# Performance work log

Measured on AMD Instinct MI355X. Metric: run time of the kernel, lower is better.

The kernel has to match this reference:

```python
import jax, jax.numpy as jnp
import numpy as np

EPS = 1e-6
LAMBDA_INIT = 0.8
ROPE_BASE = 10000.0
NUM_HEADS = 8


def rmsnorm(x, w):
    rms = jnp.sqrt(jnp.mean(x * x, axis=-1, keepdims=True) + EPS)
    return x / rms * w


def apply_rope(x):
    # Faithful to source: positions are taken along dim -2 of x.
    # Here x has shape (B, r, H, d), so rotation angle is indexed by HEAD index
    # (this mirrors the original torch code, where apply_rope is called on
    # (B, seq, H, d) tensors and uses x.shape[-2] == H for positions).
    d = x.shape[-1]
    half = d // 2  # d is even (head_dim=64)
    pos = jnp.arange(x.shape[-2])
    dim_idx = jnp.arange(half, dtype=x.dtype)
    freqs = 1.0 / (ROPE_BASE ** (dim_idx / half))
    angles = pos[:, None].astype(jnp.float32) * freqs  # (H, half)
    cos, sin = jnp.cos(angles), jnp.sin(angles)
    x1, x2 = x[..., :half], x[..., half:2 * half]
    return jnp.concatenate([x1 * cos - x2 * sin, x1 * sin + x2 * cos], axis=-1)


def linterp(x, out_size):
    # torch F.interpolate(mode='linear', align_corners=False) along axis 1 of (B, L, C)
    in_size = x.shape[1]
    scale = in_size / out_size
    coords = jnp.clip((jnp.arange(out_size) + 0.5) * scale - 0.5, 0.0, in_size - 1)
    lo = jnp.floor(coords).astype(jnp.int32)
    hi = jnp.minimum(lo + 1, in_size - 1)
    w = (coords - lo)[None, :, None].astype(x.dtype)
    return x[:, lo] * (1 - w) + x[:, hi] * w


def setup_inputs() -> dict:
    key = jax.random.key(0)
    ks = jax.random.split(key, 12)
    B, L, C = 4, 4096, 1024
    H = NUM_HEADS
    d = C // (2 * H)  # 64
    s = 0.02
    return {
        "x": jax.random.normal(ks[0], (B, L, C), jnp.float32),
        "Wq": jax.random.normal(ks[1], (C, C), jnp.float32) * s,
        "Wk": jax.random.normal(ks[2], (C, C), jnp.float32) * s,
        "Wv": jax.random.normal(ks[3], (C, C), jnp.float32) * s,
        "Wo": jax.random.normal(ks[4], (C, C), jnp.float32) * s,
        "q_norm_w": 1.0 + jax.random.normal(ks[5], (d,), jnp.float32) * s,
        "k_norm_w": 1.0 + jax.random.normal(ks[6], (d,), jnp.float32) * s,
        "head_norm_w": 1.0 + jax.random.normal(ks[7], (2 * d,), jnp.float32) * s,
        "lambda_q1": jax.random.normal(ks[8], (d,), jnp.float32) * 0.1,
        "lambda_k1": jax.random.normal(ks[9], (d,), jnp.float32) * 0.1,
        "lambda_q2": jax.random.normal(ks[10], (d,), jnp.float32) * 0.1,
        "lambda_k2": jax.random.normal(ks[11], (d,), jnp.float32) * 0.1,
    }


def reference(x, Wq, Wk, Wv, Wo, q_norm_w, k_norm_w, head_norm_w,
              lambda_q1, lambda_k1, lambda_q2, lambda_k2):
    B, L, C = x.shape
    H = NUM_HEADS
    d = C // (2 * H)
    scale = d ** -0.5
    r = max(1, int(L ** 0.75))  # 512 for L=4096

    xd = linterp(x, r)  # (B, r, C)

    q = (xd @ Wq.T).reshape(B, r, H, 2, d)
    k = (xd @ Wk.T).reshape(B, r, H, 2, d)
    v = (xd @ Wv.T).reshape(B, r, H, 2 * d)

    q1 = apply_rope(rmsnorm(q[..., 0, :], q_norm_w))
    q2 = apply_rope(rmsnorm(q[..., 1, :], q_norm_w))
    k1 = apply_rope(rmsnorm(k[..., 0, :], k_norm_w))
    k2 = apply_rope(rmsnorm(k[..., 1, :], k_norm_w))

    # (B, H, r, d)
    q1, q2 = jnp.swapaxes(q1, 1, 2), jnp.swapaxes(q2, 1, 2)
    k1, k2 = jnp.swapaxes(k1, 1, 2), jnp.swapaxes(k2, 1, 2)
    v = jnp.swapaxes(v, 1, 2)  # (B, H, r, 2d)

    lam = (jnp.exp(jnp.sum(lambda_q1 * lambda_k1))
           - jnp.exp(jnp.sum(lambda_q2 * lambda_k2)) + LAMBDA_INIT)

    attn1 = jax.nn.softmax(jnp.einsum('bhqd,bhkd->bhqk', q1, k1) * scale, axis=-1)
    attn2 = jax.nn.softmax(jnp.einsum('bhqd,bhkd->bhqk', q2, k2) * scale, axis=-1)
    diff = jnp.einsum('bhqk,bhkd->bhqd', attn1 - lam * attn2, v)  # (B,H,r,2d)

    diff = jnp.swapaxes(diff, 1, 2)  # (B, r, H, 2d)
    diff = rmsnorm(diff, head_norm_w) * (1.0 - LAMBDA_INIT)
    lowrank_out = jax.nn.silu(diff.reshape(B, r, C) @ Wo.T)
    full_out = linterp(lowrank_out, L)
    return (full_out, lowrank_out)
```

## Files before the change

### kernel.cpp

```cpp
#include <hip/hip_runtime.h>

typedef __bf16 bf16_t;
typedef __bf16 bf16x8 __attribute__((ext_vector_type(8)));
typedef __bf16 bf16x4 __attribute__((ext_vector_type(4)));
typedef float  f32x4  __attribute__((ext_vector_type(4)));

#define MFMA16(a,b,c) __builtin_amdgcn_mfma_f32_16x16x32_bf16((a),(b),(c),0,0,0)

#define NB 4
#define LL 4096
#define CC 1024
#define HH 8
#define RR 512

__global__ void k_prep(const float* __restrict__ x,
                       const float* __restrict__ w0, const float* __restrict__ w1,
                       const float* __restrict__ w2, const float* __restrict__ w3,
                       bf16_t* __restrict__ wbf, bf16_t* __restrict__ xd) {
  int bid = blockIdx.x;
  if (bid < 4096) {
    int y = bid >> 10;
    const float* src = (y == 0) ? w0 : (y == 1) ? w1 : (y == 2) ? w2 : w3;
    int idx = (bid & 1023) * 256 + threadIdx.x;
    f32x4 v = *(const f32x4*)&src[(size_t)idx * 4];
    bf16x4 o;
#pragma unroll
    for (int j = 0; j < 4; ++j) o[j] = (bf16_t)v[j];
    *(bf16x4*)&wbf[(size_t)y * 1048576 + (size_t)idx * 4] = o;
  } else {
    int idx = (bid - 4096) * 256 + threadIdx.x;
    int c4  = idx & 255;
    int row = idx >> 8;
    int b = row >> 9, i = row & 511;
    const float* p0 = x + (size_t)(b * LL + 8 * i + 3) * CC + c4 * 4;
    f32x4 a = *(const f32x4*)p0;
    f32x4 bb = *(const f32x4*)(p0 + CC);
    bf16x4 o;
#pragma unroll
    for (int j = 0; j < 4; ++j) o[j] = (bf16_t)(0.5f * (a[j] + bb[j]));
    *(bf16x4*)&xd[(size_t)row * CC + c4 * 4] = o;
  }
}

template <int CH>
__device__ __forceinline__ void stage_async(const bf16_t* __restrict__ g, bf16_t* __restrict__ s, int t) {
#pragma unroll
  for (int j = 0; j < CH; ++j) {
    int c = t + j * 256;
    const bf16_t* ga = g + (c >> 2) * 1024 + (c & 3) * 8;
    bf16_t* la = s + c * 8;
    __builtin_amdgcn_global_load_lds((const __attribute__((address_space(1))) void*)ga,
                                     (__attribute__((address_space(3))) void*)la, 16, 0, 0);
  }
}

template <int MODE, int BM>
__global__ __launch_bounds__(256) void k_gemm(const bf16_t* __restrict__ A,
                                              const bf16_t* __restrict__ wbf,
                                              const float* __restrict__ qw,
                                              const float* __restrict__ kw,
                                              bf16_t* __restrict__ q1, bf16_t* __restrict__ q2,
                                              bf16_t* __restrict__ k1, bf16_t* __restrict__ k2,
                                              bf16_t* __restrict__ vt, float* __restrict__ outF) {
  __shared__ bf16_t sA[3][BM * 32];
  __shared__ bf16_t sB[3][128 * 32];
  const int z = (MODE == 0) ? blockIdx.z : 3;
  const bf16_t* W = wbf + (size_t)z * (1u << 20);
  int t = threadIdx.x;
  int lane = t & 63, w = t >> 6;
  int wr = w >> 1, wc = w & 1;
  int lr = lane & 15, quad = lane >> 4;
  int m0 = blockIdx.y * BM, n0 = blockIdx.x * 128;
  constexpr int NI = BM / 32;
  f32x4 acc[NI][4] = {};

  const bf16_t* Ab = A + (size_t)m0 * 1024;
  const bf16_t* Wb = W + (size_t)n0 * 1024;

  stage_async<BM / 64>(Ab, sA[0], t);
  stage_async<2>(Wb, sB[0], t);
  stage_async<BM / 64>(Ab + 32, sA[1], t);
  stage_async<2>(Wb + 32, sB[1], t);

  int cur = 0, stg = 2;
#pragma unroll 1
  for (int it = 0; it < 32; ++it) {
    if (it < 31) {
      if constexpr (BM == 128) asm volatile("s_waitcnt vmcnt(4) lgkmcnt(0)" ::: "memory");
      else                     asm volatile("s_waitcnt vmcnt(3) lgkmcnt(0)" ::: "memory");
    } else {
      asm volatile("s_waitcnt vmcnt(0) lgkmcnt(0)" ::: "memory");
    }
    __builtin_amdgcn_s_barrier();
    if (it < 30) {
      stage_async<BM / 64>(Ab + (it + 2) * 32, sA[stg], t);
      stage_async<2>(Wb + (it + 2) * 32, sB[stg], t);
    }
    const bf16_t* cA = sA[cur];
    const bf16_t* cB = sB[cur];
    bf16x8 af[NI], bfr[4];
#pragma unroll
    for (int i = 0; i < NI; ++i) af[i] = *(const bf16x8*)&cA[(wr * (BM / 2) + i * 16 + lr) * 32 + quad * 8];
#pragma unroll
    for (int j = 0; j < 4; ++j) bfr[j] = *(const bf16x8*)&cB[(wc * 64 + j * 16 + lr) * 32 + quad * 8];
#pragma unroll
    for (int i = 0; i < NI; ++i)
#pragma unroll
      for (int j = 0; j < 4; ++j)
        acc[i][j] = MFMA16(af[i], bfr[j], acc[i][j]);
    cur = (cur == 2) ? 0 : cur + 1;
    stg = (stg == 2) ? 0 : stg + 1;
  }

  if (MODE == 1) {
#pragma unroll
    for (int i = 0; i < NI; ++i)
#pragma unroll
      for (int j = 0; j < 4; ++j) {
        int row0 = m0 + wr * (BM / 2) + i * 16 + quad * 4;
        int col  = n0 + wc * 64 + j * 16 + lr;
#pragma unroll
        for (int rg = 0; rg < 4; ++rg) {
          float v = acc[i][j][rg];
          outF[(size_t)(row0 + rg) * 1024 + col] = v / (1.f + __expf(-v));
        }
      }
    return;
  }

  if (z == 2) {
#pragma unroll
    for (int i = 0; i < NI; ++i)
#pragma unroll
      for (int j = 0; j < 4; ++j) {
        int row0 = m0 + wr * (BM / 2) + i * 16 + quad * 4;
        int col  = n0 + wc * 64 + j * 16 + lr;
        int b = row0 >> 9, ii = row0 & 511;
        int h = col >> 7, nn = col & 127;
        bf16x4 pk;
#pragma unroll
        for (int rg = 0; rg < 4; ++rg) pk[rg] = (bf16_t)acc[i][j][rg];
        *(bf16x4*)&vt[(size_t)((b * HH + h) * 128 + nn) * 512 + ii] = pk;
      }
    return;
  }

  {
    const float* nw = z ? kw : qw;
    int colbase = n0 + wc * 64;
    int h = colbase >> 7;
    int slot = (colbase >> 6) & 1;
    bf16_t* dst = (z == 0) ? (slot ? q2 : q1) : (slot ? k2 : k1);
    float qs = (z == 0) ? 0.125f : 1.0f;
    float w0 = nw[lr], w1 = nw[16 + lr], w2 = nw[32 + lr], w3 = nw[48 + lr];
    const float nlog = -13.287712379549449f / 32.f;
    float f0 = exp2f((float)lr * nlog);
    float f1 = exp2f((float)(16 + lr) * nlog);
    float sn0, cs0, sn1, cs1;
    __sincosf((float)h * f0, &sn0, &cs0);
    __sincosf((float)h * f1, &sn1, &cs1);
#pragma unroll
    for (int i = 0; i < NI; ++i) {
#pragma unroll
      for (int rg = 0; rg < 4; ++rg) {
        float v0 = acc[i][0][rg], v1 = acc[i][1][rg], v2 = acc[i][2][rg], v3 = acc[i][3][rg];
        float ss = v0 * v0 + v1 * v1 + v2 * v2 + v3 * v3;
#pragma unroll
        for (int m = 1; m <= 8; m <<= 1) ss += __shfl_xor(ss, m);
        float rinv = qs / sqrtf(ss * (1.f / 64.f) + 1e-6f);
        float n0v = v0 * rinv * w0, n1v = v1 * rinv * w1, n2v = v2 * rinv * w2, n3v = v3 * rinv * w3;
        float o0 = n0v * cs0 - n2v * sn0;
        float o1 = n1v * cs1 - n3v * sn1;
        float o2 = n0v * sn0 + n2v * cs0;
        float o3 = n1v * sn1 + n3v * cs1;
        int row = m0 + wr * (BM / 2) + i * 16 + quad * 4 + rg;
        int b = row >> 9, seq = row & 511;
        size_t base = ((size_t)((b * HH + h) * RR + seq)) * 64;
        dst[base + lr]      = (bf16_t)o0;
        dst[base + 16 + lr] = (bf16_t)o1;
        dst[base + 32 + lr] = (bf16_t)o2;
        dst[base + 48 + lr] = (bf16_t)o3;
      }
    }
  }
}

__global__ __launch_bounds__(256) void k_attn(const bf16_t* __restrict__ q1, const bf16_t* __restrict__ q2,
                                              const bf16_t* __restrict__ k1, const bf16_t* __restrict__ k2,
                                              const bf16_t* __restrict__ vt,
                                              const float* __restrict__ lq1, const float* __restrict__ lk1,
                                              const float* __restrict__ lq2, const float* __restrict__ lk2,
                                              const float* __restrict__ hw, bf16_t* __restrict__ anorm) {
  __shared__ bf16_t P[16 * 520];
  __shared__ float Sm1[4][16], Sl1[4][16], Sm2[4][16], Sl2[4][16], Sq[4][16];
  int t = threadIdx.x;
  int lane = t & 63, w = t >> 6;
  int lr = lane & 15, quad = lane >> 4;
  int qt = blockIdx.x, bh = blockIdx.y;
  int b = bh >> 3, h = bh & 7;

  float t1 = lq1[lane] * lk1[lane];
  float t2 = lq2[lane] * lk2[lane];
#pragma unroll
  for (int m = 1; m <= 32; m <<= 1) { t1 += __shfl_xor(t1, m); t2 += __shfl_xor(t2, m); }
  float lam = expf(t1) - expf(t2) + 0.8f;

  const bf16_t* q1b = q1 + (size_t)(bh * RR + qt * 16) * 64;
  const bf16_t* q2b = q2 + (size_t)(bh * RR + qt * 16) * 64;
  const bf16_t* k1b = k1 + (size_t)bh * RR * 64;
  const bf16_t* k2b = k2 + (size_t)bh * RR * 64;
  const bf16_t* vtb = vt + (size_t)bh * 128 * 512;

  bf16x8 a1[2], a2[2];
#pragma unroll
  for (int kk = 0; kk < 2; ++kk) {
    a1[kk] = *(const bf16x8*)&q1b[lr * 64 + kk * 32 + quad * 8];
    a2[kk] = *(const bf16x8*)&q2b[lr * 64 + kk * 32 + quad * 8];
  }

  f32x4 s1[8], s2[8];
#pragma unroll
  for (int kt = 0; kt < 8; ++kt) {
    const bf16_t* kr = k1b + (size_t)((w * 8 + kt) * 16 + lr) * 64 + quad * 8;
    f32x4 a = {};
    a = MFMA16(a1[0], *(const bf16x8*)kr, a);
    a = MFMA16(a1[1], *(const bf16x8*)(kr + 32), a);
    s1[kt] = a;
  }
#pragma unroll
  for (int kt = 0; kt < 8; ++kt) {
    const bf16_t* kr = k2b + (size_t)((w * 8 + kt) * 16 + lr) * 64 + quad * 8;
    f32x4 a = {};
    a = MFMA16(a2[0], *(const bf16x8*)kr, a);
    a = MFMA16(a2[1], *(const bf16x8*)(kr + 32), a);
    s2[kt] = a;
  }
  float m1[4] = {-3e38f, -3e38f, -3e38f, -3e38f}, m2[4] = {-3e38f, -3e38f, -3e38f, -3e38f};
#pragma unroll
  for (int kt = 0; kt < 8; ++kt)
#pragma unroll
    for (int rg = 0; rg < 4; ++rg) { m1[rg] = fmaxf(m1[rg], s1[kt][rg]); m2[rg] = fmaxf(m2[rg], s2[kt][rg]); }
#pragma unroll
  for (int m = 1; m <= 8; m <<= 1)
#pragma unroll
    for (int rg = 0; rg < 4; ++rg) { m1[rg] = fmaxf(m1[rg], __shfl_xor(m1[rg], m)); m2[rg] = fmaxf(m2[rg], __shfl_xor(m2[rg], m)); }
  float l1[4] = {}, l2[4] = {};
#pragma unroll
  for (int kt = 0; kt < 8; ++kt)
#pragma unroll
    for (int rg = 0; rg < 4; ++rg) {
      float e1 = __expf(s1[kt][rg] - m1[rg]); s1[kt][rg] = e1; l1[rg] += e1;
      float e2 = __expf(s2[kt][rg] - m2[rg]); s2[kt][rg] = e2; l2[rg] += e2;
    }
#pragma unroll
  for (int m = 1; m <= 8; m <<= 1)
#pragma unroll
    for (int rg = 0; rg < 4; ++rg) { l1[rg] += __shfl_xor(l1[rg], m); l2[rg] += __shfl_xor(l2[rg], m); }
  if (lr == 0) {
#pragma unroll
    for (int rg = 0; rg < 4; ++rg) {
      int r = quad * 4 + rg;
      Sm1[w][r] = m1[rg]; Sl1[w][r] = l1[rg];
      Sm2[w][r] = m2[rg]; Sl2[w][r] = l2[rg];
    }
  }
  __syncthreads();
  float sc1[4], sc2[4];
#pragma unroll
  for (int rg = 0; rg < 4; ++rg) {
    int r = quad * 4 + rg;
    float gm1 = fmaxf(fmaxf(Sm1[0][r], Sm1[1][r]), fmaxf(Sm1[2][r], Sm1[3][r]));
    float L1 = Sl1[0][r] * __expf(Sm1[0][r] - gm1) + Sl1[1][r] * __expf(Sm1[1][r] - gm1)
             + Sl1[2][r] * __expf(Sm1[2][r] - gm1) + Sl1[3][r] * __expf(Sm1[3][r] - gm1);
    sc1[rg] = __expf(m1[rg] - gm1) / L1;
    float gm2 = fmaxf(fmaxf(Sm2[0][r], Sm2[1][r]), fmaxf(Sm2[2][r], Sm2[3][r]));
    float L2 = Sl2[0][r] * __expf(Sm2[0][r] - gm2) + Sl2[1][r] * __expf(Sm2[1][r] - gm2)
             + Sl2[2][r] * __expf(Sm2[2][r] - gm2) + Sl2[3][r] * __expf(Sm2[3][r] - gm2);
    sc2[rg] = lam * __expf(m2[rg] - gm2) / L2;
  }
#pragma unroll
  for (int kt = 0; kt < 8; ++kt)
#pragma unroll
    for (int rg = 0; rg < 4; ++rg) {
      float v = s1[kt][rg] * sc1[rg] - s2[kt][rg] * sc2[rg];
      P[(quad * 4 + rg) * 520 + (w * 8 + kt) * 16 + lr] = (bf16_t)v;
    }
  __syncthreads();
  f32x4 accO[2] = {};
#pragma unroll
  for (int ks = 0; ks < 16; ++ks) {
    bf16x8 pf = *(bf16x8*)&P[lr * 520 + ks * 32 + quad * 8];
#pragma unroll
    for (int j = 0; j < 2; ++j) {
      int nt = w * 2 + j;
      bf16x8 vf = *(const bf16x8*)&vtb[(size_t)(nt * 16 + lr) * 512 + ks * 32 + quad * 8];
      accO[j] = MFMA16(pf, vf, accO[j]);
    }
  }
  float ssr[4] = {};
#pragma unroll
  for (int j = 0; j < 2; ++j)
#pragma unroll
    for (int rg = 0; rg < 4; ++rg) ssr[rg] += accO[j][rg] * accO[j][rg];
#pragma unroll
  for (int m = 1; m <= 8; m <<= 1)
#pragma unroll
    for (int rg = 0; rg < 4; ++rg) ssr[rg] += __shfl_xor(ssr[rg], m);
  if (lr == 0) {
#pragma unroll
    for (int rg = 0; rg < 4; ++rg) Sq[w][quad * 4 + rg] = ssr[rg];
  }
  __syncthreads();
#pragma unroll
  for (int j = 0; j < 2; ++j) {
    int nt = w * 2 + j;
    float wcol = hw[nt * 16 + lr];
#pragma unroll
    for (int rg = 0; rg < 4; ++rg) {
      int r = quad * 4 + rg;
      float tot = Sq[0][r] + Sq[1][r] + Sq[2][r] + Sq[3][r];
      float rinv = 0.2f / sqrtf(tot * (1.f / 128.f) + 1e-6f);
      int i = qt * 16 + r;
      anorm[(size_t)(b * RR + i) * 1024 + h * 128 + nt * 16 + lr] = (bf16_t)(accO[j][rg] * rinv * wcol);
    }
  }
}

__global__ void k_up(const float* __restrict__ lrk, float* __restrict__ out) {
  int j = blockIdx.x;
  int b = blockIdx.y;
  int c = threadIdx.x * 4;
  float coord = 0.125f * (float)j - 0.4375f;
  coord = fminf(fmaxf(coord, 0.f), 511.f);
  int lo = (int)floorf(coord);
  int hi = lo + 1 < 511 ? lo + 1 : 511;
  float w = coord - (float)lo;
  f32x4 a = *(const f32x4*)&lrk[(size_t)(b * RR + lo) * CC + c];
  f32x4 bb = *(const f32x4*)&lrk[(size_t)(b * RR + hi) * CC + c];
  f32x4 o;
#pragma unroll
  for (int t = 0; t < 4; ++t) o[t] = a[t] * (1.f - w) + bb[t] * w;
  *(f32x4*)&out[(size_t)(b * LL + j) * CC + c] = o;
}

extern "C" void kernel_launch(void* const* d_in, const int* in_sizes, int n_in,
                              void* d_out, int out_size, void* d_ws, size_t ws_size,
                              hipStream_t stream) {
  (void)in_sizes; (void)n_in; (void)out_size; (void)ws_size;
  const float* x   = (const float*)d_in[0];
  const float* Wq  = (const float*)d_in[1];
  const float* Wk  = (const float*)d_in[2];
  const float* Wv  = (const float*)d_in[3];
  const float* Wo  = (const float*)d_in[4];
  const float* qw  = (const float*)d_in[5];
  const float* kw  = (const float*)d_in[6];
  const float* hw  = (const float*)d_in[7];
  const float* lq1 = (const float*)d_in[8];
  const float* lk1 = (const float*)d_in[9];
  const float* lq2 = (const float*)d_in[10];
  const float* lk2 = (const float*)d_in[11];
  float* out = (float*)d_out;

  char* ws = (char*)d_ws;
  bf16_t* wbf   = (bf16_t*)(ws);
  bf16_t* xd    = (bf16_t*)(ws + (8u << 20));
  bf16_t* vt    = (bf16_t*)(ws + (12u << 20));
  bf16_t* q1    = (bf16_t*)(ws + (16u << 20));
  bf16_t* q2    = (bf16_t*)(ws + (18u << 20));
  bf16_t* k1    = (bf16_t*)(ws + (20u << 20));
  bf16_t* k2    = (bf16_t*)(ws + (22u << 20));
  bf16_t* anorm = (bf16_t*)(ws + (24u << 20));

  float* lowrank = out + (size_t)NB * LL * CC;

  k_prep<<<6144, 256, 0, stream>>>(x, Wq, Wk, Wv, Wo, wbf, xd);
  k_gemm<0, 128><<<dim3(8, 16, 3), 256, 0, stream>>>(xd, wbf, qw, kw, q1, q2, k1, k2, vt, nullptr);
  k_attn<<<dim3(32, 32), 256, 0, stream>>>(q1, q2, k1, k2, vt, lq1, lk1, lq2, lk2, hw, anorm);
  k_gemm<1, 64><<<dim3(8, 32, 1), 256, 0, stream>>>(anorm, wbf, qw, kw, nullptr, nullptr, nullptr, nullptr, nullptr, lowrank);
  k_up<<<dim3(4096, 4), 256, 0, stream>>>(lowrank, out);
}
```

Before: 237.4 us.

## Fuse all stages into one persistent kernel with grid-wide atomic barriers

Replaces the five separate launches (prep, QKV GEMM, attention, output GEMM, upsample) with a single persistent kernel of 768 blocks that loops over tasks and separates stages with a software grid barrier built on an atomic counter. The GEMM tiles are re-shaped so that each stage maps onto the fixed grid (64x128 for QKV, 64x64 for the output projection). The aim is to remove per-launch overhead and tail gaps between kernels. In exchange it relies on all 768 blocks being co-resident for the spin barrier to be safe, adds atomic polling cost, and leaves blocks idle in the stages that have fewer tasks than the grid.

```diff
diff --git a/kernel.cpp b/kernel.cpp
--- a/kernel.cpp
+++ b/kernel.cpp
@@ -12,34 +12,17 @@
 #define CC 1024
 #define HH 8
 #define RR 512
-
-__global__ void k_prep(const float* __restrict__ x,
-                       const float* __restrict__ w0, const float* __restrict__ w1,
-                       const float* __restrict__ w2, const float* __restrict__ w3,
-                       bf16_t* __restrict__ wbf, bf16_t* __restrict__ xd) {
-  int bid = blockIdx.x;
-  if (bid < 4096) {
-    int y = bid >> 10;
-    const float* src = (y == 0) ? w0 : (y == 1) ? w1 : (y == 2) ? w2 : w3;
-    int idx = (bid & 1023) * 256 + threadIdx.x;
-    f32x4 v = *(const f32x4*)&src[(size_t)idx * 4];
-    bf16x4 o;
-#pragma unroll
-    for (int j = 0; j < 4; ++j) o[j] = (bf16_t)v[j];
-    *(bf16x4*)&wbf[(size_t)y * 1048576 + (size_t)idx * 4] = o;
-  } else {
-    int idx = (bid - 4096) * 256 + threadIdx.x;
-    int c4  = idx & 255;
-    int row = idx >> 8;
-    int b = row >> 9, i = row & 511;
-    const float* p0 = x + (size_t)(b * LL + 8 * i + 3) * CC + c4 * 4;
-    f32x4 a = *(const f32x4*)p0;
-    f32x4 bb = *(const f32x4*)(p0 + CC);
-    bf16x4 o;
-#pragma unroll
-    for (int j = 0; j < 4; ++j) o[j] = (bf16_t)(0.5f * (a[j] + bb[j]));
-    *(bf16x4*)&xd[(size_t)row * CC + c4 * 4] = o;
-  }
+#define GRID 768
+
+__device__ __forceinline__ void gsync(unsigned* cnt, unsigned target) {
+  __syncthreads();
+  if (threadIdx.x == 0) {
+    __threadfence();
+    atomicAdd(cnt, 1u);
+    while (atomicAdd(cnt, 0u) < target) __builtin_amdgcn_s_sleep(8);
+    __threadfence();
+  }
+  __syncthreads();
 }
 
 template <int CH>
@@ -54,71 +37,65 @@
   }
 }
 
-template <int MODE, int BM>
-__global__ __launch_bounds__(256) void k_gemm(const bf16_t* __restrict__ A,
-                                              const bf16_t* __restrict__ wbf,
-                                              const float* __restrict__ qw,
-                                              const float* __restrict__ kw,
-                                              bf16_t* __restrict__ q1, bf16_t* __restrict__ q2,
-                                              bf16_t* __restrict__ k1, bf16_t* __restrict__ k2,
-                                              bf16_t* __restrict__ vt, float* __restrict__ outF) {
-  __shared__ bf16_t sA[3][BM * 32];
-  __shared__ bf16_t sB[3][128 * 32];
-  const int z = (MODE == 0) ? blockIdx.z : 3;
-  const bf16_t* W = wbf + (size_t)z * (1u << 20);
-  int t = threadIdx.x;
+template <int MODE, int BM, int BN>
+__device__ __forceinline__ void gemm_core(const bf16_t* __restrict__ A, const bf16_t* __restrict__ W,
+                                          const float* __restrict__ qw, const float* __restrict__ kw,
+                                          bf16_t* __restrict__ q1, bf16_t* __restrict__ q2,
+                                          bf16_t* __restrict__ k1, bf16_t* __restrict__ k2,
+                                          bf16_t* __restrict__ vt, float* __restrict__ outF,
+                                          bf16_t* sA, bf16_t* sB, int m0, int n0, int z, int t) {
   int lane = t & 63, w = t >> 6;
   int wr = w >> 1, wc = w & 1;
   int lr = lane & 15, quad = lane >> 4;
-  int m0 = blockIdx.y * BM, n0 = blockIdx.x * 128;
-  constexpr int NI = BM / 32;
-  f32x4 acc[NI][4] = {};
-
+  constexpr int NI = BM / 32, NJ = BN / 32;
+  f32x4 acc[NI][NJ] = {};
   const bf16_t* Ab = A + (size_t)m0 * 1024;
   const bf16_t* Wb = W + (size_t)n0 * 1024;
 
-  stage_async<BM / 64>(Ab, sA[0], t);
-  stage_async<2>(Wb, sB[0], t);
-  stage_async<BM / 64>(Ab + 32, sA[1], t);
-  stage_async<2>(Wb + 32, sB[1], t);
+  stage_async<BM / 64>(Ab, sA, t);
+  stage_async<BN / 64>(Wb, sB, t);
+  stage_async<BM / 64>(Ab + 32, sA + BM * 32, t);
+  stage_async<BN / 64>(Wb + 32, sB + BN * 32, t);
 
   int cur = 0, stg = 2;
 #pragma unroll 1
   for (int it = 0; it < 32; ++it) {
     if (it < 31) {
-      if constexpr (BM == 128) asm volatile("s_waitcnt vmcnt(4) lgkmcnt(0)" ::: "memory");
-      else                     asm volatile("s_waitcnt vmcnt(3) lgkmcnt(0)" ::: "memory");
+      constexpr int L = BM / 64 + BN / 64;
+      if constexpr (L == 2) asm volatile("s_waitcnt vmcnt(2) lgkmcnt(0)" ::: "memory");
+      else if constexpr (L == 3) asm volatile("s_waitcnt vmcnt(3) lgkmcnt(0)" ::: "memory");
+      else asm volatile("s_waitcnt vmcnt(4) lgkmcnt(0)" ::: "memory");
     } else {
       asm volatile("s_waitcnt vmcnt(0) lgkmcnt(0)" ::: "memory");
     }
     __builtin_amdgcn_s_barrier();
     if (it < 30) {
-      stage_async<BM / 64>(Ab + (it + 2) * 32, sA[stg], t);
-      stage_async<2>(Wb + (it + 2) * 32, sB[stg], t);
-    }
-    const bf16_t* cA = sA[cur];
-    const bf16_t* cB = sB[cur];
-    bf16x8 af[NI], bfr[4];
+      stage_async<BM / 64>(Ab + (it + 2) * 32, sA + stg * (BM * 32), t);
+      stage_async<BN / 64>(Wb + (it + 2) * 32, sB + stg * (BN * 32), t);
+    }
+    const bf16_t* cA = sA + cur * (BM * 32);
+    const bf16_t* cB = sB + cur * (BN * 32);
+    bf16x8 af[NI], bfr[NJ];
 #pragma unroll
     for (int i = 0; i < NI; ++i) af[i] = *(const bf16x8*)&cA[(wr * (BM / 2) + i * 16 + lr) * 32 + quad * 8];
 #pragma unroll
-    for (int j = 0; j < 4; ++j) bfr[j] = *(const bf16x8*)&cB[(wc * 64 + j * 16 + lr) * 32 + quad * 8];
+    for (int j = 0; j < NJ; ++j) bfr[j] = *(const bf16x8*)&cB[(wc * (BN / 2) + j * 16 + lr) * 32 + quad * 8];
 #pragma unroll
     for (int i = 0; i < NI; ++i)
 #pragma unroll
-      for (int j = 0; j < 4; ++j)
+      for (int j = 0; j < NJ; ++j)
         acc[i][j] = MFMA16(af[i], bfr[j], acc[i][j]);
     cur = (cur == 2) ? 0 : cur + 1;
     stg = (stg == 2) ? 0 : stg + 1;
   }
 
-  if (MODE == 1) {
+  if constexpr (MODE == 1) {
 #pragma unroll
     for (int i = 0; i < NI; ++i)
 #pragma unroll
-      for (int j = 0; j < 4; ++j) {
+      for (int j = 0; j < NJ; ++j) {
         int row0 = m0 + wr * (BM / 2) + i * 16 + quad * 4;
-        int col  = n0 + wc * 64 + j * 16 + lr;
+        int col  = n0 + wc * (BN / 2) + j * 16 + lr;
 #pragma unroll
         for (int rg = 0; rg < 4; ++rg) {
           float v = acc[i][j][rg];
@@ -126,28 +103,25 @@
         }
       }
     return;
-  }
-
-  if (z == 2) {
-#pragma unroll
-    for (int i = 0; i < NI; ++i)
-#pragma unroll
-      for (int j = 0; j < 4; ++j) {
-        int row0 = m0 + wr * (BM / 2) + i * 16 + quad * 4;
-        int col  = n0 + wc * 64 + j * 16 + lr;
-        int b = row0 >> 9, ii = row0 & 511;
-        int h = col >> 7, nn = col & 127;
-        bf16x4 pk;
-#pragma unroll
-        for (int rg = 0; rg < 4; ++rg) pk[rg] = (bf16_t)acc[i][j][rg];
-        *(bf16x4*)&vt[(size_t)((b * HH + h) * 128 + nn) * 512 + ii] = pk;
-      }
-    return;
-  }
-
-  {
+  } else {
+    if (z == 2) {
+#pragma unroll
+      for (int i = 0; i < NI; ++i)
+#pragma unroll
+        for (int j = 0; j < NJ; ++j) {
+          int row0 = m0 + wr * (BM / 2) + i * 16 + quad * 4;
+          int col  = n0 + wc * (BN / 2) + j * 16 + lr;
+          int b = row0 >> 9, ii = row0 & 511;
+          int h = col >> 7, nn = col & 127;
+          bf16x4 pk;
+#pragma unroll
+          for (int rg = 0; rg < 4; ++rg) pk[rg] = (bf16_t)acc[i][j][rg];
+          *(bf16x4*)&vt[(size_t)((b * HH + h) * 128 + nn) * 512 + ii] = pk;
+        }
+      return;
+    }
     const float* nw = z ? kw : qw;
-    int colbase = n0 + wc * 64;
+    int colbase = n0 + wc * (BN / 2);
     int h = colbase >> 7;
     int slot = (colbase >> 6) & 1;
     bf16_t* dst = (z == 0) ? (slot ? q2 : q1) : (slot ? k2 : k1);
@@ -185,162 +159,220 @@
   }
 }
 
-__global__ __launch_bounds__(256) void k_attn(const bf16_t* __restrict__ q1, const bf16_t* __restrict__ q2,
-                                              const bf16_t* __restrict__ k1, const bf16_t* __restrict__ k2,
-                                              const bf16_t* __restrict__ vt,
-                                              const float* __restrict__ lq1, const float* __restrict__ lk1,
-                                              const float* __restrict__ lq2, const float* __restrict__ lk2,
-                                              const float* __restrict__ hw, bf16_t* __restrict__ anorm) {
-  __shared__ bf16_t P[16 * 520];
-  __shared__ float Sm1[4][16], Sl1[4][16], Sm2[4][16], Sl2[4][16], Sq[4][16];
+__global__ __launch_bounds__(256, 3) void mega(
+    const float* __restrict__ x,
+    const float* __restrict__ Wq, const float* __restrict__ Wk,
+    const float* __restrict__ Wv, const float* __restrict__ Wo,
+    const float* __restrict__ qw, const float* __restrict__ kw,
+    const float* __restrict__ hw,
+    const float* __restrict__ lq1, const float* __restrict__ lk1,
+    const float* __restrict__ lq2, const float* __restrict__ lk2,
+    bf16_t* __restrict__ wbf, bf16_t* __restrict__ xd, bf16_t* __restrict__ vt,
+    bf16_t* __restrict__ q1, bf16_t* __restrict__ q2,
+    bf16_t* __restrict__ k1, bf16_t* __restrict__ k2,
+    bf16_t* __restrict__ anorm, float* __restrict__ lowrank,
+    float* __restrict__ out, unsigned* cnt) {
+  __shared__ __align__(16) char smem[36864];
+  bf16_t* sA = (bf16_t*)smem;
+  bf16_t* sB = (bf16_t*)(smem + 12288);
   int t = threadIdx.x;
-  int lane = t & 63, w = t >> 6;
+  int bid = blockIdx.x;
+  int lane = t & 63, wv = t >> 6;
   int lr = lane & 15, quad = lane >> 4;
-  int qt = blockIdx.x, bh = blockIdx.y;
-  int b = bh >> 3, h = bh & 7;
-
-  float t1 = lq1[lane] * lk1[lane];
-  float t2 = lq2[lane] * lk2[lane];
-#pragma unroll
-  for (int m = 1; m <= 32; m <<= 1) { t1 += __shfl_xor(t1, m); t2 += __shfl_xor(t2, m); }
-  float lam = expf(t1) - expf(t2) + 0.8f;
-
-  const bf16_t* q1b = q1 + (size_t)(bh * RR + qt * 16) * 64;
-  const bf16_t* q2b = q2 + (size_t)(bh * RR + qt * 16) * 64;
-  const bf16_t* k1b = k1 + (size_t)bh * RR * 64;
-  const bf16_t* k2b = k2 + (size_t)bh * RR * 64;
-  const bf16_t* vtb = vt + (size_t)bh * 128 * 512;
-
-  bf16x8 a1[2], a2[2];
-#pragma unroll
-  for (int kk = 0; kk < 2; ++kk) {
-    a1[kk] = *(const bf16x8*)&q1b[lr * 64 + kk * 32 + quad * 8];
-    a2[kk] = *(const bf16x8*)&q2b[lr * 64 + kk * 32 + quad * 8];
-  }
-
-  f32x4 s1[8], s2[8];
-#pragma unroll
-  for (int kt = 0; kt < 8; ++kt) {
-    const bf16_t* kr = k1b + (size_t)((w * 8 + kt) * 16 + lr) * 64 + quad * 8;
-    f32x4 a = {};
-    a = MFMA16(a1[0], *(const bf16x8*)kr, a);
-    a = MFMA16(a1[1], *(const bf16x8*)(kr + 32), a);
-    s1[kt] = a;
-  }
-#pragma unroll
-  for (int kt = 0; kt < 8; ++kt) {
-    const bf16_t* kr = k2b + (size_t)((w * 8 + kt) * 16 + lr) * 64 + quad * 8;
-    f32x4 a = {};
-    a = MFMA16(a2[0], *(const bf16x8*)kr, a);
-    a = MFMA16(a2[1], *(const bf16x8*)(kr + 32), a);
-    s2[kt] = a;
-  }
-  float m1[4] = {-3e38f, -3e38f, -3e38f, -3e38f}, m2[4] = {-3e38f, -3e38f, -3e38f, -3e38f};
-#pragma unroll
-  for (int kt = 0; kt < 8; ++kt)
-#pragma unroll
-    for (int rg = 0; rg < 4; ++rg) { m1[rg] = fmaxf(m1[rg], s1[kt][rg]); m2[rg] = fmaxf(m2[rg], s2[kt][rg]); }
-#pragma unroll
-  for (int m = 1; m <= 8; m <<= 1)
-#pragma unroll
-    for (int rg = 0; rg < 4; ++rg) { m1[rg] = fmaxf(m1[rg], __shfl_xor(m1[rg], m)); m2[rg] = fmaxf(m2[rg], __shfl_xor(m2[rg], m)); }
-  float l1[4] = {}, l2[4] = {};
-#pragma unroll
-  for (int kt = 0; kt < 8; ++kt)
-#pragma unroll
-    for (int rg = 0; rg < 4; ++rg) {
-      float e1 = __expf(s1[kt][rg] - m1[rg]); s1[kt][rg] = e1; l1[rg] += e1;
-      float e2 = __expf(s2[kt][rg] - m2[rg]); s2[kt][rg] = e2; l2[rg] += e2;
-    }
-#pragma unroll
-  for (int m = 1; m <= 8; m <<= 1)
-#pragma unroll
-    for (int rg = 0; rg < 4; ++rg) { l1[rg] += __shfl_xor(l1[rg], m); l2[rg] += __shfl_xor(l2[rg], m); }
-  if (lr == 0) {
-#pragma unroll
-    for (int rg = 0; rg < 4; ++rg) {
-      int r = quad * 4 + rg;
-      Sm1[w][r] = m1[rg]; Sl1[w][r] = l1[rg];
-      Sm2[w][r] = m2[rg]; Sl2[w][r] = l2[rg];
-    }
-  }
-  __syncthreads();
-  float sc1[4], sc2[4];
-#pragma unroll
-  for (int rg = 0; rg < 4; ++rg) {
-    int r = quad * 4 + rg;
-    float gm1 = fmaxf(fmaxf(Sm1[0][r], Sm1[1][r]), fmaxf(Sm1[2][r], Sm1[3][r]));
-    float L1 = Sl1[0][r] * __expf(Sm1[0][r] - gm1) + Sl1[1][r] * __expf(Sm1[1][r] - gm1)
-             + Sl1[2][r] * __expf(Sm1[2][r] - gm1) + Sl1[3][r] * __expf(Sm1[3][r] - gm1);
-    sc1[rg] = __expf(m1[rg] - gm1) / L1;
-    float gm2 = fmaxf(fmaxf(Sm2[0][r], Sm2[1][r]), fmaxf(Sm2[2][r], Sm2[3][r]));
-    float L2 = Sl2[0][r] * __expf(Sm2[0][r] - gm2) + Sl2[1][r] * __expf(Sm2[1][r] - gm2)
-             + Sl2[2][r] * __expf(Sm2[2][r] - gm2) + Sl2[3][r] * __expf(Sm2[3][r] - gm2);
-    sc2[rg] = lam * __expf(m2[rg] - gm2) / L2;
-  }
-#pragma unroll
-  for (int kt = 0; kt < 8; ++kt)
-#pragma unroll
-    for (int rg = 0; rg < 4; ++rg) {
-      float v = s1[kt][rg] * sc1[rg] - s2[kt][rg] * sc2[rg];
-      P[(quad * 4 + rg) * 520 + (w * 8 + kt) * 16 + lr] = (bf16_t)v;
-    }
-  __syncthreads();
-  f32x4 accO[2] = {};
-#pragma unroll
-  for (int ks = 0; ks < 16; ++ks) {
-    bf16x8 pf = *(bf16x8*)&P[lr * 520 + ks * 32 + quad * 8];
-#pragma unroll
-    for (int j = 0; j < 2; ++j) {
-      int nt = w * 2 + j;
-      bf16x8 vf = *(const bf16x8*)&vtb[(size_t)(nt * 16 + lr) * 512 + ks * 32 + quad * 8];
-      accO[j] = MFMA16(pf, vf, accO[j]);
-    }
-  }
-  float ssr[4] = {};
-#pragma unroll
-  for (int j = 0; j < 2; ++j)
-#pragma unroll
-    for (int rg = 0; rg < 4; ++rg) ssr[rg] += accO[j][rg] * accO[j][rg];
-#pragma unroll
-  for (int m = 1; m <= 8; m <<= 1)
-#pragma unroll
-    for (int rg = 0; rg < 4; ++rg) ssr[rg] += __shfl_xor(ssr[rg], m);
-  if (lr == 0) {
-#pragma unroll
-    for (int rg = 0; rg < 4; ++rg) Sq[w][quad * 4 + rg] = ssr[rg];
-  }
-  __syncthreads();
-#pragma unroll
-  for (int j = 0; j < 2; ++j) {
-    int nt = w * 2 + j;
-    float wcol = hw[nt * 16 + lr];
-#pragma unroll
-    for (int rg = 0; rg < 4; ++rg) {
-      int r = quad * 4 + rg;
-      float tot = Sq[0][r] + Sq[1][r] + Sq[2][r] + Sq[3][r];
-      float rinv = 0.2f / sqrtf(tot * (1.f / 128.f) + 1e-6f);
-      int i = qt * 16 + r;
-      anorm[(size_t)(b * RR + i) * 1024 + h * 128 + nt * 16 + lr] = (bf16_t)(accO[j][rg] * rinv * wcol);
-    }
-  }
-}
-
-__global__ void k_up(const float* __restrict__ lrk, float* __restrict__ out) {
-  int j = blockIdx.x;
-  int b = blockIdx.y;
-  int c = threadIdx.x * 4;
-  float coord = 0.125f * (float)j - 0.4375f;
-  coord = fminf(fmaxf(coord, 0.f), 511.f);
-  int lo = (int)floorf(coord);
-  int hi = lo + 1 < 511 ? lo + 1 : 511;
-  float w = coord - (float)lo;
-  f32x4 a = *(const f32x4*)&lrk[(size_t)(b * RR + lo) * CC + c];
-  f32x4 bb = *(const f32x4*)&lrk[(size_t)(b * RR + hi) * CC + c];
-  f32x4 o;
-#pragma unroll
-  for (int t = 0; t < 4; ++t) o[t] = a[t] * (1.f - w) + bb[t] * w;
-  *(f32x4*)&out[(size_t)(b * LL + j) * CC + c] = o;
+
+  for (int task = bid; task < 6144; task += GRID) {
+    if (task < 4096) {
+      int y = task >> 10;
+      const float* src = (y == 0) ? Wq : (y == 1) ? Wk : (y == 2) ? Wv : Wo;
+      int idx = (task & 1023) * 256 + t;
+      f32x4 v = *(const f32x4*)&src[(size_t)idx * 4];
+      bf16x4 o;
+#pragma unroll
+      for (int j = 0; j < 4; ++j) o[j] = (bf16_t)v[j];
+      *(bf16x4*)&wbf[(size_t)y * 1048576 + (size_t)idx * 4] = o;
+    } else {
+      int idx = (task - 4096) * 256 + t;
+      int c4  = idx & 255;
+      int row = idx >> 8;
+      int b = row >> 9, i = row & 511;
+      const float* p0 = x + (size_t)(b * LL + 8 * i + 3) * CC + c4 * 4;
+      f32x4 a = *(const f32x4*)p0;
+      f32x4 bb = *(const f32x4*)(p0 + CC);
+      bf16x4 o;
+#pragma unroll
+      for (int j = 0; j < 4; ++j) o[j] = (bf16_t)(0.5f * (a[j] + bb[j]));
+      *(bf16x4*)&xd[(size_t)row * CC + c4 * 4] = o;
+    }
+  }
+  gsync(cnt, GRID);
+
+  {
+    int z = bid >> 8, rem = bid & 255;
+    int n0 = (rem & 7) * 128, m0 = (rem >> 3) * 64;
+    gemm_core<0, 64, 128>(xd, wbf + (size_t)z * (1u << 20), qw, kw,
+                          q1, q2, k1, k2, vt, nullptr, sA, sB, m0, n0, z, t);
+  }
+  gsync(cnt, 2 * GRID);
+
+  {
+    bf16_t* P   = (bf16_t*)smem;
+    float* Sf   = (float*)(smem + 16640);
+    float* Sm1 = Sf, *Sl1 = Sf + 64, *Sm2 = Sf + 128, *Sl2 = Sf + 192, *Sq = Sf + 256;
+
+    float t1 = lq1[lane] * lk1[lane];
+    float t2 = lq2[lane] * lk2[lane];
+#pragma unroll
+    for (int m = 1; m <= 32; m <<= 1) { t1 += __shfl_xor(t1, m); t2 += __shfl_xor(t2, m); }
+    float lam = expf(t1) - expf(t2) + 0.8f;
+
+    for (int task = bid; task < 1024; task += GRID) {
+      int qt = task & 31, bh = task >> 5;
+      int b = bh >> 3, h = bh & 7;
+      const bf16_t* q1b = q1 + (size_t)(bh * RR + qt * 16) * 64;
+      const bf16_t* q2b = q2 + (size_t)(bh * RR + qt * 16) * 64;
+      const bf16_t* k1b = k1 + (size_t)bh * RR * 64;
+      const bf16_t* k2b = k2 + (size_t)bh * RR * 64;
+      const bf16_t* vtb = vt + (size_t)bh * 128 * 512;
+
+      bf16x8 a1[2], a2[2];
+#pragma unroll
+      for (int kk = 0; kk < 2; ++kk) {
+        a1[kk] = *(const bf16x8*)&q1b[lr * 64 + kk * 32 + quad * 8];
+        a2[kk] = *(const bf16x8*)&q2b[lr * 64 + kk * 32 + quad * 8];
+      }
+      f32x4 s1[8], s2[8];
+#pragma unroll
+      for (int kt = 0; kt < 8; ++kt) {
+        const bf16_t* kr = k1b + (size_t)((wv * 8 + kt) * 16 + lr) * 64 + quad * 8;
+        f32x4 a = {};
+        a = MFMA16(a1[0], *(const bf16x8*)kr, a);
+        a = MFMA16(a1[1], *(const bf16x8*)(kr + 32), a);
+        s1[kt] = a;
+      }
+#pragma unroll
+      for (int kt = 0; kt < 8; ++kt) {
+        const bf16_t* kr = k2b + (size_t)((wv * 8 + kt) * 16 + lr) * 64 + quad * 8;
+        f32x4 a = {};
+        a = MFMA16(a2[0], *(const bf16x8*)kr, a);
+        a = MFMA16(a2[1], *(const bf16x8*)(kr + 32), a);
+        s2[kt] = a;
+      }
+      float m1[4] = {-3e38f, -3e38f, -3e38f, -3e38f}, m2[4] = {-3e38f, -3e38f, -3e38f, -3e38f};
+#pragma unroll
+      for (int kt = 0; kt < 8; ++kt)
+#pragma unroll
+        for (int rg = 0; rg < 4; ++rg) { m1[rg] = fmaxf(m1[rg], s1[kt][rg]); m2[rg] = fmaxf(m2[rg], s2[kt][rg]); }
+#pragma unroll
+      for (int m = 1; m <= 8; m <<= 1)
+#pragma unroll
+        for (int rg = 0; rg < 4; ++rg) { m1[rg] = fmaxf(m1[rg], __shfl_xor(m1[rg], m)); m2[rg] = fmaxf(m2[rg], __shfl_xor(m2[rg], m)); }
+      float l1[4] = {}, l2[4] = {};
+#pragma unroll
+      for (int kt = 0; kt < 8; ++kt)
+#pragma unroll
+        for (int rg = 0; rg < 4; ++rg) {
+          float e1 = __expf(s1[kt][rg] - m1[rg]); s1[kt][rg] = e1; l1[rg] += e1;
+          float e2 = __expf(s2[kt][rg] - m2[rg]); s2[kt][rg] = e2; l2[rg] += e2;
+        }
+#pragma unroll
+      for (int m = 1; m <= 8; m <<= 1)
+#pragma unroll
+        for (int rg = 0; rg < 4; ++rg) { l1[rg] += __shfl_xor(l1[rg], m); l2[rg] += __shfl_xor(l2[rg], m); }
+      if (lr == 0) {
+#pragma unroll
+        for (int rg = 0; rg < 4; ++rg) {
+          int r = quad * 4 + rg;
+          Sm1[wv * 16 + r] = m1[rg]; Sl1[wv * 16 + r] = l1[rg];
+          Sm2[wv * 16 + r] = m2[rg]; Sl2[wv * 16 + r] = l2[rg];
+        }
+      }
+      __syncthreads();
+      float sc1[4], sc2[4];
+#pragma unroll
+      for (int rg = 0; rg < 4; ++rg) {
+        int r = quad * 4 + rg;
+        float gm1 = fmaxf(fmaxf(Sm1[r], Sm1[16 + r]), fmaxf(Sm1[32 + r], Sm1[48 + r]));
+        float L1 = Sl1[r] * __expf(Sm1[r] - gm1) + Sl1[16 + r] * __expf(Sm1[16 + r] - gm1)
+                 + Sl1[32 + r] * __expf(Sm1[32 + r] - gm1) + Sl1[48 + r] * __expf(Sm1[48 + r] - gm1);
+        sc1[rg] = __expf(m1[rg] - gm1) / L1;
+        float gm2 = fmaxf(fmaxf(Sm2[r], Sm2[16 + r]), fmaxf(Sm2[32 + r], Sm2[48 + r]));
+        float L2 = Sl2[r] * __expf(Sm2[r] - gm2) + Sl2[16 + r] * __expf(Sm2[16 + r] - gm2)
+                 + Sl2[32 + r] * __expf(Sm2[32 + r] - gm2) + Sl2[48 + r] * __expf(Sm2[48 + r] - gm2);
+        sc2[rg] = lam * __expf(m2[rg] - gm2) / L2;
+      }
+#pragma unroll
+      for (int kt = 0; kt < 8; ++kt)
+#pragma unroll
+        for (int rg = 0; rg < 4; ++rg) {
+          float v = s1[kt][rg] * sc1[rg] - s2[kt][rg] * sc2[rg];
+          P[(quad * 4 + rg) * 520 + (wv * 8 + kt) * 16 + lr] = (bf16_t)v;
+        }
+      __syncthreads();
+      f32x4 accO[2] = {};
+#pragma unroll
+      for (int ks = 0; ks < 16; ++ks) {
+        bf16x8 pf = *(bf16x8*)&P[lr * 520 + ks * 32 + quad * 8];
+#pragma unroll
+        for (int j = 0; j < 2; ++j) {
+          int nt = wv * 2 + j;
+          bf16x8 vf = *(const bf16x8*)&vtb[(size_t)(nt * 16 + lr) * 512 + ks * 32 + quad * 8];
+          accO[j] = MFMA16(pf, vf, accO[j]);
+        }
+      }
+      float ssr[4] = {};
+#pragma unroll
+      for (int j = 0; j < 2; ++j)
+#pragma unroll
+        for (int rg = 0; rg < 4; ++rg) ssr[rg] += accO[j][rg] * accO[j][rg];
+#pragma unroll
+      for (int m = 1; m <= 8; m <<= 1)
+#pragma unroll
+        for (int rg = 0; rg < 4; ++rg) ssr[rg] += __shfl_xor(ssr[rg], m);
+      if (lr == 0) {
+#pragma unroll
+        for (int rg = 0; rg < 4; ++rg) Sq[wv * 16 + quad * 4 + rg] = ssr[rg];
+      }
+      __syncthreads();
+#pragma unroll
+      for (int j = 0; j < 2; ++j) {
+        int nt = wv * 2 + j;
+        float wcol = hw[nt * 16 + lr];
+#pragma unroll
+        for (int rg = 0; rg < 4; ++rg) {
+          int r = quad * 4 + rg;
+          float tot = Sq[r] + Sq[16 + r] + Sq[32 + r] + Sq[48 + r];
+          float rinv = 0.2f / sqrtf(tot * (1.f / 128.f) + 1e-6f);
+          int i = qt * 16 + r;
+          anorm[(size_t)(b * RR + i) * 1024 + h * 128 + nt * 16 + lr] = (bf16_t)(accO[j][rg] * rinv * wcol);
+        }
+      }
+    }
+  }
+  gsync(cnt, 3 * GRID);
+
+  if (bid < 512) {
+    int n0 = (bid & 15) * 64, m0 = (bid >> 4) * 64;
+    gemm_core<1, 64, 64>(anorm, wbf + (size_t)3 * (1u << 20), qw, kw,
+                         nullptr, nullptr, nullptr, nullptr, nullptr, lowrank,
+                         sA, sB, m0, n0, 3, t);
+  }
+  gsync(cnt, 4 * GRID);
+
+  for (int task = bid; task < 16384; task += GRID) {
+    int j = task & 4095, b = task >> 12;
+    int c = t * 4;
+    float coord = 0.125f * (float)j - 0.4375f;
+    coord = fminf(fmaxf(coord, 0.f), 511.f);
+    int lo = (int)floorf(coord);
+    int hi = lo + 1 < 511 ? lo + 1 : 511;
+    float wt = coord - (float)lo;
+    f32x4 a = *(const f32x4*)&lowrank[(size_t)(b * RR + lo) * CC + c];
+    f32x4 bb = *(const f32x4*)&lowrank[(size_t)(b * RR + hi) * CC + c];
+    f32x4 o;
+#pragma unroll
+    for (int q = 0; q < 4; ++q) o[q] = a[q] * (1.f - wt) + bb[q] * wt;
+    *(f32x4*)&out[(size_t)(b * LL + j) * CC + c] = o;
+  }
 }
 
 extern "C" void kernel_launch(void* const* d_in, const int* in_sizes, int n_in,
@@ -370,12 +402,11 @@
   bf16_t* k1    = (bf16_t*)(ws + (20u << 20));
   bf16_t* k2    = (bf16_t*)(ws + (22u << 20));
   bf16_t* anorm = (bf16_t*)(ws + (24u << 20));
+  unsigned* cnt = (unsigned*)(ws + (28u << 20));
 
   float* lowrank = out + (size_t)NB * LL * CC;
 
-  k_prep<<<6144, 256, 0, stream>>>(x, Wq, Wk, Wv, Wo, wbf, xd);
-  k_gemm<0, 128><<<dim3(8, 16, 3), 256, 0, stream>>>(xd, wbf, qw, kw, q1, q2, k1, k2, vt, nullptr);
-  k_attn<<<dim3(32, 32), 256, 0, stream>>>(q1, q2, k1, k2, vt, lq1, lk1, lq2, lk2, hw, anorm);
-  k_gemm<1, 64><<<dim3(8, 32, 1), 256, 0, stream>>>(anorm, wbf, qw, kw, nullptr, nullptr, nullptr, nullptr, nullptr, lowrank);
-  k_up<<<dim3(4096, 4), 256, 0, stream>>>(lowrank, out);
+  hipMemsetAsync(cnt, 0, 4, stream);
+  mega<<<GRID, 256, 0, stream>>>(x, Wq, Wk, Wv, Wo, qw, kw, hw, lq1, lk1, lq2, lk2,
+                                 wbf, xd, vt, q1, q2, k1, k2, anorm, lowrank, out, cnt);
 }
```

Result: slower. 585.0 us (+146.4%).
